# Optimization experiments

Hardware: AMD Instinct MI355X
Metric: run time of the kernel (lower is better)

The kernel has to match this reference:

```python
import jax, jax.numpy as jnp
import numpy as np

B, T, I, H, L = 10, 2048, 128, 256, 6


def setup_inputs() -> dict:
    key = jax.random.key(0)
    ks = jax.random.split(key, 8)
    k = 1.0 / np.sqrt(H)  # PyTorch LSTM init: U(-1/sqrt(H), 1/sqrt(H))
    u = lambda kk, shape: jax.random.uniform(kk, shape, jnp.float32, -k, k)
    return {
        "x": jax.random.normal(ks[0], (B, T, I), jnp.float32),
        "h0": jax.random.normal(ks[1], (L, B, H), jnp.float32),
        "c0": jax.random.normal(ks[2], (L, B, H), jnp.float32),
        "W_ih0": u(ks[3], (4 * H, I)),          # layer 0 input weights
        "W_ih": u(ks[4], (L - 1, 4 * H, H)),    # layers 1..5 input weights
        "W_hh": u(ks[5], (L, 4 * H, H)),
        "b_ih": u(ks[6], (L, 4 * H)),
        "b_hh": u(ks[7], (L, 4 * H)),
    }


def _lstm_layer(seq, h0, c0, Wih, Whh, bih, bhh):
    """seq: [B,T,F] -> (out_seq [B,T,H], cT [B,H]). PyTorch gate order i,f,g,o."""
    # Precompute input contribution for all timesteps in one GEMM.
    x_gates = jnp.einsum("btf,gf->btg", seq, Wih) + bih + bhh  # [B,T,4H]

    def step(carry, xg):  # xg: [B,4H]
        h, c = carry
        g = xg + h @ Whh.T
        i, f, gg, o = jnp.split(g, 4, axis=-1)
        c = jax.nn.sigmoid(f) * c + jax.nn.sigmoid(i) * jnp.tanh(gg)
        h = jax.nn.sigmoid(o) * jnp.tanh(c)
        return (h, c), h

    (hT, cT), hs = jax.lax.scan(step, (h0, c0), jnp.swapaxes(x_gates, 0, 1))
    return jnp.swapaxes(hs, 0, 1), cT


def reference(x, h0, c0, W_ih0, W_ih, W_hh, b_ih, b_hh):
    seq = x
    c_finals = []
    for l in range(L):
        Wih = W_ih0 if l == 0 else W_ih[l - 1]
        seq, cT = _lstm_layer(seq, h0[l], c0[l], Wih, W_hh[l], b_ih[l], b_hh[l])
        c_finals.append(cT)
    return jnp.stack(c_finals)  # [L,B,H] = state[1] (c_n)
```

## Files before the change

### kernel.cpp

```cpp
#include <hip/hip_runtime.h>

#define LAYERS 6
#define BB 10
#define TT 2048
#define II 128
#define HH 256
#define GPL 32
#define DEPTH 8
#define NTH 256
#define NROW 32
#define HCSTR 520
#define PSTR 392
#define SLOTU 1280
#define NCOL 8

typedef unsigned long long u64;
typedef unsigned int u32;

struct __align__(16) Smem {
    float hc[BB][HCSTR];
    float red[4][PSTR];
    float cst[NCOL][BB];
    float bias_s[NROW];
};

__device__ __forceinline__ float fsig(float x) { return 1.0f / (1.0f + __expf(-x)); }
__device__ __forceinline__ float ftanh(float x) {
    x = fminf(fmaxf(x, -15.0f), 15.0f);
    float e = __expf(2.0f * x);
    return (e - 1.0f) / (e + 1.0f);
}
__device__ __forceinline__ int ld_cnt(const int* p) {
    return __hip_atomic_load(p, __ATOMIC_RELAXED, __HIP_MEMORY_SCOPE_AGENT);
}
__device__ __forceinline__ void st_cnt(int* p, int v) {
    __hip_atomic_store(p, v, __ATOMIC_RELAXED, __HIP_MEMORY_SCOPE_AGENT);
}
__device__ __forceinline__ u64 ld_u64(const u64* p) {
    return __hip_atomic_load(p, __ATOMIC_RELAXED, __HIP_MEMORY_SCOPE_AGENT);
}
__device__ __forceinline__ void st_u64(u64* p, u64 v) {
    __hip_atomic_store(p, v, __ATOMIC_RELAXED, __HIP_MEMORY_SCOPE_AGENT);
}
__device__ __forceinline__ u32 bf16r(float v) {
    u32 x = __float_as_uint(v);
    return (x + 0x7FFFu + ((x >> 16) & 1u)) >> 16;
}
__device__ __forceinline__ u64 packh(float h0, float h1, u32 tag) {
    return ((u64)tag << 32) | ((u64)bf16r(h0) << 16) | (u64)bf16r(h1);
}
__device__ __forceinline__ float2 unpackh(u64 v) {
    return make_float2(__uint_as_float(((u32)(v >> 16) & 0xFFFFu) << 16),
                       __uint_as_float(((u32)v & 0xFFFFu) << 16));
}
__device__ __forceinline__ int div40(int u) { return (int)(((unsigned)u * 52429u) >> 21); }

template <int CTRL>
__device__ __forceinline__ float dpp_xadd(float v) {
    int t = __builtin_amdgcn_mov_dpp(__float_as_int(v), CTRL, 0xf, 0xf, true);
    return v + __int_as_float(t);
}
__device__ __forceinline__ void poll32(const int* base, int tgt, bool sleep) {
    const int lane = threadIdx.x & 63;
    const int* p = base + (lane & 31);
    for (;;) {
        int v = ld_cnt(p);
        if (__ballot((lane < 32) && (v < tgt)) == 0) break;
        if (sleep) __builtin_amdgcn_s_sleep(2);
    }
    asm volatile("" ::: "memory");
}

template <int CH4>
__device__ void run_layer(Smem& sm, int l, int s,
                          const float* __restrict__ x,
                          const float* __restrict__ h0,
                          const float* __restrict__ c0,
                          const float* __restrict__ Wih0,
                          const float* __restrict__ Wih,
                          const float* __restrict__ Whh,
                          const float* __restrict__ bih,
                          const float* __restrict__ bhh,
                          float* __restrict__ out,
                          int* flags, float* hring)
{
    constexpr int K = CH4 * 128;
    constexpr int F = K - HH;
    constexpr int XC = CH4 - 2;
    const int tid  = threadIdx.x;
    const int kc   = tid & 31;
    const int rg   = tid >> 5;
    const int wave = tid >> 6;

    const float* WihL = (F == II) ? Wih0 : (Wih + (size_t)(l - 1) * 4 * HH * HH);
    const float* WhhL = Whh + (size_t)l * 4 * HH * HH;

    float4 wreg[4][CH4];
    #pragma unroll
    for (int ri = 0; ri < 4; ++ri) {
        const int rloc = rg * 4 + ri;
        const int gr = (rloc >> 3) * HH + s * NCOL + (rloc & 7);
        #pragma unroll
        for (int i4 = 0; i4 < CH4; ++i4) {
            const int k0 = (i4 * 32 + kc) * 4;
            float tmp[4];
            #pragma unroll
            for (int c = 0; c < 4; ++c) {
                const int kk = k0 + c;
                tmp[c] = (kk < F) ? WihL[(size_t)gr * F + kk]
                                  : WhhL[(size_t)gr * HH + (kk - F)];
            }
            wreg[ri][i4] = make_float4(tmp[0], tmp[1], tmp[2], tmp[3]);
        }
    }
    if (tid < NROW) {
        const int gr = (tid >> 3) * HH + s * NCOL + (tid & 7);
        sm.bias_s[tid] = bih[l * 4 * HH + gr] + bhh[l * 4 * HH + gr];
    }
    if (tid < NCOL * BB) {
        const int j = tid & 7, b = tid >> 3;
        sm.cst[j][b] = c0[((size_t)l * BB + b) * HH + s * NCOL + j];
    }

    u64* const ringu  = (u64*)(hring + (size_t)l * DEPTH * BB * HH);
    const u64* belowu = (const u64*)(hring + (size_t)(l - 1) * DEPTH * BB * HH);

    if (F == II) {
        #pragma unroll
        for (int i = 0; i < 2; ++i) {
            const int q = tid + i * NTH;
            if (q < BB * (II / 4))
                *(float4*)&sm.hc[q >> 5][(q & 31) * 4] =
                    *(const float4*)&x[((size_t)(q >> 5) * TT + 0) * II + (q & 31) * 4];
        }
    } else {
        u64 v[5];
        #pragma unroll
        for (int i = 0; i < 5; ++i) v[i] = ld_u64(belowu + tid + i * NTH);
        for (;;) {
            bool bad = false;
            #pragma unroll
            for (int i = 0; i < 5; ++i) bad |= ((u32)(v[i] >> 32) != 1u);
            if (__ballot(bad) == 0) break;
            __builtin_amdgcn_s_sleep(2);
            #pragma unroll
            for (int i = 0; i < 5; ++i) v[i] = ld_u64(belowu + tid + i * NTH);
        }
        asm volatile("" ::: "memory");
        #pragma unroll
        for (int i = 0; i < 5; ++i) {
            const int u = tid + i * NTH, sp = div40(u), q = u - 40 * sp;
            *(float2*)&sm.hc[q >> 2][sp * 8 + (q & 3) * 2] = unpackh(v[i]);
        }
    }
    __syncthreads();

    u64 pk = 0;

    for (int t = 0; t < TT; ++t) {
        if (t > 0 && tid < 40)
            st_u64(ringu + (size_t)((t - 1) & (DEPTH - 1)) * SLOTU + s * 40 + tid, pk);
        if (F != II && t > 0 && tid == 64) st_cnt(&flags[l * 32 + s], t);

        u64 cv[5];
        const u64* ownslot = ringu + (size_t)((t - 1) & (DEPTH - 1)) * SLOTU;
        if (t > 0) {
            #pragma unroll
            for (int i = 0; i < 5; ++i) cv[i] = ld_u64(ownslot + tid + i * NTH);
        }

        float acc[4][BB];
        #pragma unroll
        for (int ri = 0; ri < 4; ++ri)
            #pragma unroll
            for (int b = 0; b < BB; ++b) acc[ri][b] = 0.0f;

        #pragma unroll
        for (int i4 = 0; i4 < XC; ++i4) {
            const int col = (i4 * 32 + kc) * 4;
            #pragma unroll
            for (int b = 0; b < BB; ++b) {
                const float4 h4 = *(const float4*)&sm.hc[b][col];
                #pragma unroll
                for (int ri = 0; ri < 4; ++ri) {
                    acc[ri][b] = fmaf(wreg[ri][i4].x, h4.x, acc[ri][b]);
                    acc[ri][b] = fmaf(wreg[ri][i4].y, h4.y, acc[ri][b]);
                    acc[ri][b] = fmaf(wreg[ri][i4].z, h4.z, acc[ri][b]);
                    acc[ri][b] = fmaf(wreg[ri][i4].w, h4.w, acc[ri][b]);
                }
            }
        }

        if (t > 0) {
            const u32 tg = (u32)t;
            for (;;) {
                bool bad = false;
                #pragma unroll
                for (int i = 0; i < 5; ++i) bad |= ((u32)(cv[i] >> 32) != tg);
                if (__ballot(bad) == 0) break;
                #pragma unroll
                for (int i = 0; i < 5; ++i) cv[i] = ld_u64(ownslot + tid + i * NTH);
            }
            asm volatile("" ::: "memory");
            #pragma unroll
            for (int i = 0; i < 5; ++i) {
                const int u = tid + i * NTH, sp = div40(u), q = u - 40 * sp;
                *(float2*)&sm.hc[q >> 2][F + sp * 8 + (q & 3) * 2] = unpackh(cv[i]);
            }
        } else {
            const u64* src = (const u64*)(h0 + (size_t)l * BB * HH);
            u64 v[5];
            #pragma unroll
            for (int i = 0; i < 5; ++i) v[i] = ld_u64(src + tid + i * NTH);
            #pragma unroll
            for (int i = 0; i < 5; ++i) {
                const int f = 2 * (tid + i * NTH);
                union { u64 u; float2 f2; } c; c.u = v[i];
                *(float2*)&sm.hc[f >> 8][F + (f & 255)] = c.f2;
            }
        }
        __syncthreads();

        #pragma unroll
        for (int i4 = XC; i4 < CH4; ++i4) {
            const int col = (i4 * 32 + kc) * 4;
            #pragma unroll
            for (int b = 0; b < BB; ++b) {
                const float4 h4 = *(const float4*)&sm.hc[b][col];
                #pragma unroll
                for (int ri = 0; ri < 4; ++ri) {
                    acc[ri][b] = fmaf(wreg[ri][i4].x, h4.x, acc[ri][b]);
                    acc[ri][b] = fmaf(wreg[ri][i4].y, h4.y, acc[ri][b]);
                    acc[ri][b] = fmaf(wreg[ri][i4].z, h4.z, acc[ri][b]);
                    acc[ri][b] = fmaf(wreg[ri][i4].w, h4.w, acc[ri][b]);
                }
            }
        }
        #pragma unroll
        for (int ri = 0; ri < 4; ++ri)
            #pragma unroll
            for (int b = 0; b < BB; ++b) {
                float v = acc[ri][b];
                v = dpp_xadd<0xB1>(v);
                v = dpp_xadd<0x4E>(v);
                v = dpp_xadd<0x128>(v);
                acc[ri][b] = v;
            }
        if ((kc & 0x0B) == 0) {
            const int p = ((kc >> 2) & 1) | ((kc >> 3) & 2);
            float* dst = &sm.red[p][(rg * 4) * 12];
            #pragma unroll
            for (int ri = 0; ri < 4; ++ri) {
                *(float4*)&dst[ri * 12 + 0] =
                    make_float4(acc[ri][0], acc[ri][1], acc[ri][2], acc[ri][3]);
                *(float4*)&dst[ri * 12 + 4] =
                    make_float4(acc[ri][4], acc[ri][5], acc[ri][6], acc[ri][7]);
                *(float2*)&dst[ri * 12 + 8] = make_float2(acc[ri][8], acc[ri][9]);
            }
        }
        __syncthreads();

        if (wave == 0) {
            if (t == TT - 1 && l < LAYERS - 1) poll32(flags + (l + 1) * 32, TT - 8, true);
            if (tid < 40) {
                const int b = tid >> 2, j = (tid & 3) * 2;
                float cc0, cc1, hh0, hh1;
                #pragma unroll
                for (int e = 0; e < 2; ++e) {
                    const int jj = j + e;
                    float g4[4];
                    #pragma unroll
                    for (int g = 0; g < 4; ++g) {
                        const int col = (g * 8 + jj) * 12 + b;
                        g4[g] = ((sm.red[0][col] + sm.red[1][col])
                               + (sm.red[2][col] + sm.red[3][col])) + sm.bias_s[g * 8 + jj];
                    }
                    float c = sm.cst[jj][b];
                    c = fsig(g4[1]) * c + fsig(g4[0]) * ftanh(g4[2]);
                    const float h = fsig(g4[3]) * ftanh(c);
                    sm.cst[jj][b] = c;
                    if (e == 0) { cc0 = c; hh0 = h; } else { cc1 = c; hh1 = h; }
                }
                if (t == TT - 1) {
                    if (l < LAYERS - 1)
                        st_u64(ringu + (size_t)(t & (DEPTH - 1)) * SLOTU + s * 40 + tid,
                               packh(hh0, hh1, (u32)(t + 1)));
                    *(float2*)&out[((size_t)l * BB + b) * HH + s * NCOL + j] =
                        make_float2(cc0, cc1);
                } else {
                    pk = packh(hh0, hh1, (u32)(t + 1));
                }
            }
        } else if (t + 1 < TT) {
            if (wave == 3 && l < LAYERS - 1 && t >= 8)
                poll32(flags + (l + 1) * 32, t - 7, true);
            if (F == II) {
                const int base = tid - 64;
                #pragma unroll
                for (int i = 0; i < 2; ++i) {
                    const int q = base + i * 192;
                    if (q < BB * (II / 4))
                        *(float4*)&sm.hc[q >> 5][(q & 31) * 4] =
                            *(const float4*)&x[((size_t)(q >> 5) * TT + (t + 1)) * II + (q & 31) * 4];
                }
            } else {
                const u64* src = belowu + (size_t)((t + 1) & (DEPTH - 1)) * SLOTU;
                const int base = tid - 64;
                const u32 tg = (u32)(t + 2);
                u64 v[7];
                #pragma unroll
                for (int i = 0; i < 7; ++i) {
                    const int u = base + i * 192;
                    v[i] = (u < SLOTU) ? ld_u64(src + u) : ((u64)tg << 32);
                }
                for (;;) {
                    bool bad = false;
                    #pragma unroll
                    for (int i = 0; i < 7; ++i) bad |= ((u32)(v[i] >> 32) != tg);
                    if (__ballot(bad) == 0) break;
                    __builtin_amdgcn_s_sleep(2);
                    #pragma unroll
                    for (int i = 0; i < 7; ++i) {
                        const int u = base + i * 192;
                        if (u < SLOTU) v[i] = ld_u64(src + u);
                    }
                }
                asm volatile("" ::: "memory");
                #pragma unroll
                for (int i = 0; i < 7; ++i) {
                    const int u = base + i * 192;
                    if (u < SLOTU) {
                        const int sp = div40(u), q = u - 40 * sp;
                        *(float2*)&sm.hc[q >> 2][sp * 8 + (q & 3) * 2] = unpackh(v[i]);
                    }
                }
            }
        }
        __syncthreads();
    }
}

__global__ __launch_bounds__(NTH, 1)
void lstm_persistent(const float* __restrict__ x, const float* __restrict__ h0,
                     const float* __restrict__ c0, const float* __restrict__ Wih0,
                     const float* __restrict__ Wih, const float* __restrict__ Whh,
                     const float* __restrict__ bih, const float* __restrict__ bhh,
                     float* __restrict__ out, int* flags, float* hring)
{
    __shared__ Smem sm;
    const int l = blockIdx.x / GPL;
    const int s = blockIdx.x % GPL;
    if (l == 0)
        run_layer<3>(sm, l, s, x, h0, c0, Wih0, Wih, Whh, bih, bhh, out, flags, hring);
    else
        run_layer<4>(sm, l, s, x, h0, c0, Wih0, Wih, Whh, bih, bhh, out, flags, hring);
}

extern "C" void kernel_launch(void* const* d_in, const int* in_sizes, int n_in,
                              void* d_out, int out_size, void* d_ws, size_t ws_size,
                              hipStream_t stream) {
    const float* x    = (const float*)d_in[0];
    const float* h0   = (const float*)d_in[1];
    const float* c0   = (const float*)d_in[2];
    const float* Wih0 = (const float*)d_in[3];
    const float* Wih  = (const float*)d_in[4];
    const float* Whh  = (const float*)d_in[5];
    const float* bih  = (const float*)d_in[6];
    const float* bhh  = (const float*)d_in[7];
    float* out  = (float*)d_out;

    int*   flags = (int*)d_ws;
    float* hring = (float*)((char*)d_ws + 16384);
    (void)hipMemsetAsync(d_ws, 0, 16384, stream);
    hipLaunchKernelGGL(lstm_persistent, dim3(LAYERS * GPL), dim3(NTH), 0, stream,
                       x, h0, c0, Wih0, Wih, Whh, bih, bhh, out, flags, hring);
}
```

Baseline: 7.793 ms.

## Distribute gate epilogue across all waves and prefetch next inputs early

Moves the gate nonlinearity and state update from wave 0 to 20 lanes in each of the four waves, keeps the cell state and bias in registers, and removes one block barrier per timestep. Each block now writes its h slice straight to the ring right after the epilogue instead of deferring the store to the next step. Loads from the layer below and the backpressure flag poll are issued at the top of the step so they overlap with the GEMV, and the ring layout switches to a batch-interleaved ordering. It removes the serial epilogue bottleneck and one sync per step, but adds register pressure and changes the cross-layer protocol in ways that could race.

Result: slower. 8.323 ms (+6.8%).

```diff
diff --git a/kernel.cpp b/kernel.cpp
--- a/kernel.cpp
+++ b/kernel.cpp
@@ -8,20 +8,17 @@
 #define GPL 32
 #define DEPTH 8
 #define NTH 256
-#define NROW 32
-#define HCSTR 520
-#define PSTR 392
+#define NCOL 8
+#define HCSTR 524
+#define RSTRD 52
 #define SLOTU 1280
-#define NCOL 8
 
 typedef unsigned long long u64;
 typedef unsigned int u32;
 
 struct __align__(16) Smem {
     float hc[BB][HCSTR];
-    float red[4][PSTR];
-    float cst[NCOL][BB];
-    float bias_s[NROW];
+    float red[32][RSTRD];
 };
 
 __device__ __forceinline__ float fsig(float x) { return 1.0f / (1.0f + __expf(-x)); }
@@ -46,14 +43,14 @@
     u32 x = __float_as_uint(v);
     return (x + 0x7FFFu + ((x >> 16) & 1u)) >> 16;
 }
-__device__ __forceinline__ u64 packh(float h0, float h1, u32 tag) {
-    return ((u64)tag << 32) | ((u64)bf16r(h0) << 16) | (u64)bf16r(h1);
+__device__ __forceinline__ u64 packh(float he, float ho, u32 tag) {
+    return ((u64)tag << 32) | ((u64)bf16r(he) << 16) | (u64)bf16r(ho);
 }
 __device__ __forceinline__ float2 unpackh(u64 v) {
     return make_float2(__uint_as_float(((u32)(v >> 16) & 0xFFFFu) << 16),
                        __uint_as_float(((u32)v & 0xFFFFu) << 16));
 }
-__device__ __forceinline__ int div40(int u) { return (int)(((unsigned)u * 52429u) >> 21); }
+__device__ __forceinline__ int div10(int u) { return (int)(((unsigned)u * 6554u) >> 16); }
 
 template <int CTRL>
 __device__ __forceinline__ float dpp_xadd(float v) {
@@ -91,6 +88,7 @@
     const int kc   = tid & 31;
     const int rg   = tid >> 5;
     const int wave = tid >> 6;
+    const int wl   = tid & 63;
 
     const float* WihL = (F == II) ? Wih0 : (Wih + (size_t)(l - 1) * 4 * HH * HH);
     const float* WhhL = Whh + (size_t)l * 4 * HH * HH;
@@ -98,8 +96,7 @@
     float4 wreg[4][CH4];
     #pragma unroll
     for (int ri = 0; ri < 4; ++ri) {
-        const int rloc = rg * 4 + ri;
-        const int gr = (rloc >> 3) * HH + s * NCOL + (rloc & 7);
+        const int gr = ri * HH + s * NCOL + rg;
         #pragma unroll
         for (int i4 = 0; i4 < CH4; ++i4) {
             const int k0 = (i4 * 32 + kc) * 4;
@@ -113,13 +110,17 @@
             wreg[ri][i4] = make_float4(tmp[0], tmp[1], tmp[2], tmp[3]);
         }
     }
-    if (tid < NROW) {
-        const int gr = (tid >> 3) * HH + s * NCOL + (tid & 7);
-        sm.bias_s[tid] = bih[l * 4 * HH + gr] + bhh[l * 4 * HH + gr];
-    }
-    if (tid < NCOL * BB) {
-        const int j = tid & 7, b = tid >> 3;
-        sm.cst[j][b] = c0[((size_t)l * BB + b) * HH + s * NCOL + j];
+
+    const bool gl = (wl < 20);
+    const int  gb = wl >> 1, ge = wl & 1;
+    const int  gj = 2 * wave + ge;
+    const int  gcol = s * NCOL + gj;
+    float cst = 0.0f, bi[4] = {0, 0, 0, 0};
+    if (gl) {
+        cst = c0[((size_t)l * BB + gb) * HH + gcol];
+        #pragma unroll
+        for (int g = 0; g < 4; ++g)
+            bi[g] = bih[l * 4 * HH + g * HH + gcol] + bhh[l * 4 * HH + g * HH + gcol];
     }
 
     u64* const ringu  = (u64*)(hring + (size_t)l * DEPTH * BB * HH);
@@ -149,25 +150,33 @@
         asm volatile("" ::: "memory");
         #pragma unroll
         for (int i = 0; i < 5; ++i) {
-            const int u = tid + i * NTH, sp = div40(u), q = u - 40 * sp;
-            *(float2*)&sm.hc[q >> 2][sp * 8 + (q & 3) * 2] = unpackh(v[i]);
+            const int u = tid + i * NTH, cp = div10(u), b = u - 10 * cp;
+            *(float2*)&sm.hc[b][2 * cp] = unpackh(v[i]);
         }
     }
     __syncthreads();
 
-    u64 pk = 0;
-
     for (int t = 0; t < TT; ++t) {
-        if (t > 0 && tid < 40)
-            st_u64(ringu + (size_t)((t - 1) & (DEPTH - 1)) * SLOTU + s * 40 + tid, pk);
-        if (F != II && t > 0 && tid == 64) st_cnt(&flags[l * 32 + s], t);
-
-        u64 cv[5];
+        u64 cv[5], bv[5];
         const u64* ownslot = ringu + (size_t)((t - 1) & (DEPTH - 1)) * SLOTU;
         if (t > 0) {
             #pragma unroll
             for (int i = 0; i < 5; ++i) cv[i] = ld_u64(ownslot + tid + i * NTH);
-        }
+        } else {
+            const u64* hz = (const u64*)(h0 + (size_t)l * BB * HH);
+            #pragma unroll
+            for (int i = 0; i < 5; ++i) cv[i] = ld_u64(hz + tid + i * NTH);
+        }
+        const bool haveb = (F != II) && (t + 1 < TT);
+        const u64* bslot = belowu + (size_t)((t + 1) & (DEPTH - 1)) * SLOTU;
+        if (haveb) {
+            #pragma unroll
+            for (int i = 0; i < 5; ++i) bv[i] = ld_u64(bslot + tid + i * NTH);
+        }
+        const bool bpn = (l < LAYERS - 1) && (t >= DEPTH);
+        int bp = 0x7fffffff;
+        if (bpn && wl < 32) bp = ld_cnt(&flags[(l + 1) * 32 + wl]);
+        if (F != II && t > 0 && tid == 64) st_cnt(&flags[l * 32 + s], t);
 
         float acc[4][BB];
         #pragma unroll
@@ -204,19 +213,15 @@
             asm volatile("" ::: "memory");
             #pragma unroll
             for (int i = 0; i < 5; ++i) {
-                const int u = tid + i * NTH, sp = div40(u), q = u - 40 * sp;
-                *(float2*)&sm.hc[q >> 2][F + sp * 8 + (q & 3) * 2] = unpackh(cv[i]);
+                const int u = tid + i * NTH, cp = div10(u), b = u - 10 * cp;
+                *(float2*)&sm.hc[b][F + 2 * cp] = unpackh(cv[i]);
             }
         } else {
-            const u64* src = (const u64*)(h0 + (size_t)l * BB * HH);
-            u64 v[5];
-            #pragma unroll
-            for (int i = 0; i < 5; ++i) v[i] = ld_u64(src + tid + i * NTH);
             #pragma unroll
             for (int i = 0; i < 5; ++i) {
-                const int f = 2 * (tid + i * NTH);
-                union { u64 u; float2 f2; } c; c.u = v[i];
-                *(float2*)&sm.hc[f >> 8][F + (f & 255)] = c.f2;
+                const int u = tid + i * NTH, b = u >> 7, c2 = u & 127;
+                union { u64 u_; float2 f; } cc; cc.u_ = cv[i];
+                *(float2*)&sm.hc[b][F + 2 * c2] = cc.f;
             }
         }
         __syncthreads();
@@ -236,6 +241,7 @@
                 }
             }
         }
+
         #pragma unroll
         for (int ri = 0; ri < 4; ++ri)
             #pragma unroll
@@ -246,9 +252,10 @@
                 v = dpp_xadd<0x128>(v);
                 acc[ri][b] = v;
             }
+
         if ((kc & 0x0B) == 0) {
             const int p = ((kc >> 2) & 1) | ((kc >> 3) & 2);
-            float* dst = &sm.red[p][(rg * 4) * 12];
+            float* dst = &sm.red[rg * 4 + p][0];
             #pragma unroll
             for (int ri = 0; ri < 4; ++ri) {
                 *(float4*)&dst[ri * 12 + 0] =
@@ -258,82 +265,55 @@
                 *(float2*)&dst[ri * 12 + 8] = make_float2(acc[ri][8], acc[ri][9]);
             }
         }
-        __syncthreads();
-
-        if (wave == 0) {
-            if (t == TT - 1 && l < LAYERS - 1) poll32(flags + (l + 1) * 32, TT - 8, true);
-            if (tid < 40) {
-                const int b = tid >> 2, j = (tid & 3) * 2;
-                float cc0, cc1, hh0, hh1;
-                #pragma unroll
-                for (int e = 0; e < 2; ++e) {
-                    const int jj = j + e;
-                    float g4[4];
-                    #pragma unroll
-                    for (int g = 0; g < 4; ++g) {
-                        const int col = (g * 8 + jj) * 12 + b;
-                        g4[g] = ((sm.red[0][col] + sm.red[1][col])
-                               + (sm.red[2][col] + sm.red[3][col])) + sm.bias_s[g * 8 + jj];
-                    }
-                    float c = sm.cst[jj][b];
-                    c = fsig(g4[1]) * c + fsig(g4[0]) * ftanh(g4[2]);
-                    const float h = fsig(g4[3]) * ftanh(c);
-                    sm.cst[jj][b] = c;
-                    if (e == 0) { cc0 = c; hh0 = h; } else { cc1 = c; hh1 = h; }
-                }
-                if (t == TT - 1) {
-                    if (l < LAYERS - 1)
-                        st_u64(ringu + (size_t)(t & (DEPTH - 1)) * SLOTU + s * 40 + tid,
-                               packh(hh0, hh1, (u32)(t + 1)));
-                    *(float2*)&out[((size_t)l * BB + b) * HH + s * NCOL + j] =
-                        make_float2(cc0, cc1);
-                } else {
-                    pk = packh(hh0, hh1, (u32)(t + 1));
-                }
-            }
-        } else if (t + 1 < TT) {
-            if (wave == 3 && l < LAYERS - 1 && t >= 8)
-                poll32(flags + (l + 1) * 32, t - 7, true);
-            if (F == II) {
-                const int base = tid - 64;
-                #pragma unroll
-                for (int i = 0; i < 2; ++i) {
-                    const int q = base + i * 192;
-                    if (q < BB * (II / 4))
-                        *(float4*)&sm.hc[q >> 5][(q & 31) * 4] =
-                            *(const float4*)&x[((size_t)(q >> 5) * TT + (t + 1)) * II + (q & 31) * 4];
-                }
-            } else {
-                const u64* src = belowu + (size_t)((t + 1) & (DEPTH - 1)) * SLOTU;
-                const int base = tid - 64;
-                const u32 tg = (u32)(t + 2);
-                u64 v[7];
-                #pragma unroll
-                for (int i = 0; i < 7; ++i) {
-                    const int u = base + i * 192;
-                    v[i] = (u < SLOTU) ? ld_u64(src + u) : ((u64)tg << 32);
-                }
-                for (;;) {
-                    bool bad = false;
-                    #pragma unroll
-                    for (int i = 0; i < 7; ++i) bad |= ((u32)(v[i] >> 32) != tg);
-                    if (__ballot(bad) == 0) break;
-                    __builtin_amdgcn_s_sleep(2);
-                    #pragma unroll
-                    for (int i = 0; i < 7; ++i) {
-                        const int u = base + i * 192;
-                        if (u < SLOTU) v[i] = ld_u64(src + u);
-                    }
-                }
-                asm volatile("" ::: "memory");
-                #pragma unroll
-                for (int i = 0; i < 7; ++i) {
-                    const int u = base + i * 192;
-                    if (u < SLOTU) {
-                        const int sp = div40(u), q = u - 40 * sp;
-                        *(float2*)&sm.hc[q >> 2][sp * 8 + (q & 3) * 2] = unpackh(v[i]);
-                    }
-                }
+
+        if (bpn && __ballot(bp < t - DEPTH + 1))
+            poll32(&flags[(l + 1) * 32], t - DEPTH + 1, false);
+
+        float hout = 0.0f;
+        if (gl) {
+            float g4[4];
+            #pragma unroll
+            for (int g = 0; g < 4; ++g)
+                g4[g] = ((sm.red[gj * 4 + 0][g * 12 + gb] + sm.red[gj * 4 + 1][g * 12 + gb])
+                       + (sm.red[gj * 4 + 2][g * 12 + gb] + sm.red[gj * 4 + 3][g * 12 + gb]))
+                       + bi[g];
+            float c = fsig(g4[1]) * cst + fsig(g4[0]) * ftanh(g4[2]);
+            hout = fsig(g4[3]) * ftanh(c);
+            cst = c;
+        }
+        {
+            int hp = __builtin_amdgcn_mov_dpp(__float_as_int(hout), 0xB1, 0xf, 0xf, true);
+            if (gl && ge == 0)
+                st_u64(ringu + (size_t)(t & (DEPTH - 1)) * SLOTU + (s * 4 + wave) * 10 + gb,
+                       packh(hout, __int_as_float(hp), (u32)(t + 1)));
+        }
+        if (t == TT - 1 && gl)
+            out[((size_t)l * BB + gb) * HH + gcol] = cst;
+
+        if (haveb) {
+            const u32 tg = (u32)(t + 2);
+            for (;;) {
+                bool bad = false;
+                #pragma unroll
+                for (int i = 0; i < 5; ++i) bad |= ((u32)(bv[i] >> 32) != tg);
+                if (__ballot(bad) == 0) break;
+                __builtin_amdgcn_s_sleep(1);
+                #pragma unroll
+                for (int i = 0; i < 5; ++i) bv[i] = ld_u64(bslot + tid + i * NTH);
+            }
+            asm volatile("" ::: "memory");
+            #pragma unroll
+            for (int i = 0; i < 5; ++i) {
+                const int u = tid + i * NTH, cp = div10(u), b = u - 10 * cp;
+                *(float2*)&sm.hc[b][2 * cp] = unpackh(bv[i]);
+            }
+        } else if (F == II && t + 1 < TT) {
+            #pragma unroll
+            for (int i = 0; i < 2; ++i) {
+                const int q = tid + i * NTH;
+                if (q < BB * (II / 4))
+                    *(float4*)&sm.hc[q >> 5][(q & 31) * 4] =
+                        *(const float4*)&x[((size_t)(q >> 5) * TT + (t + 1)) * II + (q & 31) * 4];
             }
         }
         __syncthreads();
```
